# Kernel optimization log

Measured on AMD Instinct MI355X. Metric: run time of the kernel, lower is better.

Reference implementation:

```python
import jax, jax.numpy as jnp
import numpy as np

B, S, D_MODEL = 2, 2048, 1024
NUM_HEADS, ATTN_DIM = 16, 64


def setup_inputs() -> dict:
    key = jax.random.key(0)
    ks = jax.random.split(key, 9)
    scale = 1.0 / np.sqrt(D_MODEL)
    states = jax.random.normal(ks[0], (B, S, D_MODEL), dtype=jnp.float32)
    Wq = jax.random.normal(ks[1], (D_MODEL, NUM_HEADS * ATTN_DIM), dtype=jnp.float32) * scale
    bq = jnp.zeros((NUM_HEADS * ATTN_DIM,), dtype=jnp.float32)
    Wk = jax.random.normal(ks[2], (D_MODEL, NUM_HEADS * ATTN_DIM), dtype=jnp.float32) * scale
    bk = jnp.zeros((NUM_HEADS * ATTN_DIM,), dtype=jnp.float32)
    Wv = jax.random.normal(ks[3], (D_MODEL, NUM_HEADS * ATTN_DIM), dtype=jnp.float32) * scale
    bv = jnp.zeros((NUM_HEADS * ATTN_DIM,), dtype=jnp.float32)
    Wo = jax.random.normal(ks[4], (NUM_HEADS * ATTN_DIM, D_MODEL), dtype=jnp.float32) * scale
    bo = jnp.zeros((D_MODEL,), dtype=jnp.float32)
    return {"states": states, "Wq": Wq, "bq": bq, "Wk": Wk, "bk": bk,
            "Wv": Wv, "bv": bv, "Wo": Wo, "bo": bo}


def reference(states, Wq, bq, Wk, bk, Wv, bv, Wo, bo):
    b, s, _ = states.shape
    h, d = NUM_HEADS, ATTN_DIM

    def proj(W, bias):
        # tanh-activated Dense, then split heads: [b, s, h*d] -> [b, h, s, d]
        y = jnp.tanh(states @ W + bias)
        return y.reshape(b, s, h, d).transpose(0, 2, 1, 3)

    q, k, v = proj(Wq, bq), proj(Wk, bk), proj(Wv, bv)
    # scores: [b, h, s, s]
    alpha = jnp.einsum("bhqd,bhkd->bhqk", q, k) / jnp.sqrt(jnp.float32(d))
    # causal mask (row i attends to cols 0..i); masked logits set to float32.min
    causal = jnp.tril(jnp.ones((s, s), dtype=bool))
    alpha = jnp.where(causal, alpha, jnp.finfo(jnp.float32).min)
    alpha = jax.nn.softmax(alpha, axis=-1)
    ctx = jnp.einsum("bhqk,bhkd->bhqd", alpha, v)  # [b, h, s, d]
    ctx = ctx.transpose(0, 2, 1, 3).reshape(b, s, h * d)
    return jnp.tanh(ctx @ Wo + bo)
```

## Files before the change

kernel.cpp:

```cpp
#include <hip/hip_runtime.h>
#include <math.h>

typedef unsigned short u16;
typedef __attribute__((ext_vector_type(4))) float f32x4;
typedef __attribute__((ext_vector_type(16))) float f32x16;
typedef __attribute__((ext_vector_type(8))) short bf16x8;

#define B_ 2
#define S_ 2048
#define DM 1024
#define H_ 16
#define AD 64
#define ME 4194304
#define SC 0.18033688011112042f
#define SMAX 12.0f

#define GLL(g, s) __builtin_amdgcn_global_load_lds( \
  (const __attribute__((address_space(1))) void*)(g), \
  (__attribute__((address_space(3))) void*)(s), 16, 0, 0)

__device__ inline u16 f2bf(float f) {
  union { float f; unsigned u; } v; v.f = f;
  unsigned r = v.u + 0x7fffu + ((v.u >> 16) & 1u);
  return (u16)(r >> 16);
}

__device__ inline unsigned cvt_pk_bf16(float lo, float hi) {
  unsigned r;
  asm("v_cvt_pk_bf16_f32 %0, %1, %2" : "=v"(r) : "v"(lo), "v"(hi));
  return r;
}

__global__ __launch_bounds__(256) void conv_states(const float* __restrict__ in,
                                                   u16* __restrict__ out) {
  int i = (blockIdx.x * 256 + threadIdx.x) * 8;
  const float4* p = (const float4*)(in + i);
  float4 a = p[0], b = p[1];
  bf16x8 o;
  o[0] = (short)f2bf(a.x); o[1] = (short)f2bf(a.y);
  o[2] = (short)f2bf(a.z); o[3] = (short)f2bf(a.w);
  o[4] = (short)f2bf(b.x); o[5] = (short)f2bf(b.y);
  o[6] = (short)f2bf(b.z); o[7] = (short)f2bf(b.w);
  *(bf16x8*)&out[i] = o;
}

__global__ void transpose_w(const float* __restrict__ Wq, const float* __restrict__ Wk,
                            const float* __restrict__ Wv, const float* __restrict__ Wo,
                            u16* __restrict__ Wt) {
  __shared__ float t[32][33];
  int z = blockIdx.z;
  const float* W = (z == 0) ? Wq : (z == 1) ? Wk : (z == 2) ? Wv : Wo;
  u16* out = Wt + (size_t)z * DM * DM;
  int n0 = blockIdx.x * 32, k0 = blockIdx.y * 32;
  int tx = threadIdx.x, ty = threadIdx.y;
  t[ty][tx] = W[(k0 + ty) * DM + n0 + tx];
  __syncthreads();
  out[(n0 + ty) * DM + k0 + tx] = f2bf(t[tx][ty]);
}

__global__ __launch_bounds__(256) void qkv_gemm(
    const u16* __restrict__ A, const u16* __restrict__ Wt,
    const float* __restrict__ bq, const float* __restrict__ bk, const float* __restrict__ bv,
    u16* __restrict__ Qw, u16* __restrict__ Kw, u16* __restrict__ Vtw) {
  __shared__ __attribute__((aligned(16))) u16 lA[128 * 32];
  __shared__ __attribute__((aligned(16))) u16 lB[128 * 32];
  const int z = blockIdx.z;
  const u16* Bt = Wt + (size_t)z * DM * DM;
  const int m0 = blockIdx.y * 128, n0 = blockIdx.x * 128;
  const int tid = threadIdx.x;
  const int wid = tid >> 6, l = tid & 63;
  const int lr = l & 15, lk = l >> 4;
  const int wm = (wid >> 1) * 64, wn = (wid & 1) * 64;
  const int srow = wid * 32 + (l >> 2);
  const int scol = (l & 3) * 8;

  f32x4 acc[4][4] = {};

  for (int k0 = 0; k0 < DM; k0 += 32) {
    const u16* gA = &A[(size_t)(m0 + srow) * DM + k0 + scol];
    const u16* gB = &Bt[(size_t)(n0 + srow) * DM + k0 + scol];
    GLL(gA,           lA + wid * 1024);
    GLL(gA + 16 * DM, lA + wid * 1024 + 512);
    GLL(gB,           lB + wid * 1024);
    GLL(gB + 16 * DM, lB + wid * 1024 + 512);
    __syncthreads();
    bf16x8 af[4], bfr[4];
#pragma unroll
    for (int g = 0; g < 4; ++g) {
      af[g]  = *(const bf16x8*)&lA[(wm + g * 16 + lr) * 32 + lk * 8];
      bfr[g] = *(const bf16x8*)&lB[(wn + g * 16 + lr) * 32 + lk * 8];
    }
#pragma unroll
    for (int mg = 0; mg < 4; ++mg)
#pragma unroll
      for (int ng = 0; ng < 4; ++ng)
        acc[mg][ng] = __builtin_amdgcn_mfma_f32_16x16x32_bf16(af[mg], bfr[ng], acc[mg][ng], 0, 0, 0);
    __syncthreads();
  }

  const float* bias = (z == 0) ? bq : (z == 1) ? bk : bv;
#pragma unroll
  for (int mg = 0; mg < 4; ++mg)
#pragma unroll
    for (int ng = 0; ng < 4; ++ng)
#pragma unroll
      for (int r = 0; r < 4; ++r) {
        int m = m0 + wm + mg * 16 + lk * 4 + r;
        int n = n0 + wn + ng * 16 + lr;
        float v = tanhf(acc[mg][ng][r] + bias[n]);
        if (z == 0) v *= SC;
        u16 h16 = f2bf(v);
        int bb = m >> 11, s = m & 2047, hh = n >> 6, d = n & 63;
        if (z == 2) Vtw[((size_t)(bb * H_ + hh) * AD + d) * S_ + s] = h16;
        else ((z == 0) ? Qw : Kw)[((size_t)(bb * H_ + hh) * S_ + s) * AD + d] = h16;
      }
}

__global__ __launch_bounds__(256) void out_gemm(
    const u16* __restrict__ A, const u16* __restrict__ Bt,
    const float* __restrict__ bo, float* __restrict__ out) {
  __shared__ __attribute__((aligned(16))) u16 lA[128 * 32];
  __shared__ __attribute__((aligned(16))) u16 lB[128 * 32];
  const int m0 = blockIdx.y * 128, n0 = blockIdx.x * 128;
  const int tid = threadIdx.x;
  const int wid = tid >> 6, l = tid & 63;
  const int lr = l & 15, lk = l >> 4;
  const int wm = (wid >> 1) * 64, wn = (wid & 1) * 64;
  const int srow = wid * 32 + (l >> 2);
  const int scol = (l & 3) * 8;

  f32x4 acc[4][4] = {};

  for (int k0 = 0; k0 < DM; k0 += 32) {
    const u16* gA = &A[(size_t)(m0 + srow) * DM + k0 + scol];
    const u16* gB = &Bt[(size_t)(n0 + srow) * DM + k0 + scol];
    GLL(gA,           lA + wid * 1024);
    GLL(gA + 16 * DM, lA + wid * 1024 + 512);
    GLL(gB,           lB + wid * 1024);
    GLL(gB + 16 * DM, lB + wid * 1024 + 512);
    __syncthreads();
    bf16x8 af[4], bfr[4];
#pragma unroll
    for (int g = 0; g < 4; ++g) {
      af[g]  = *(const bf16x8*)&lA[(wm + g * 16 + lr) * 32 + lk * 8];
      bfr[g] = *(const bf16x8*)&lB[(wn + g * 16 + lr) * 32 + lk * 8];
    }
#pragma unroll
    for (int mg = 0; mg < 4; ++mg)
#pragma unroll
      for (int ng = 0; ng < 4; ++ng)
        acc[mg][ng] = __builtin_amdgcn_mfma_f32_16x16x32_bf16(af[mg], bfr[ng], acc[mg][ng], 0, 0, 0);
    __syncthreads();
  }

#pragma unroll
  for (int mg = 0; mg < 4; ++mg)
#pragma unroll
    for (int ng = 0; ng < 4; ++ng)
#pragma unroll
      for (int r = 0; r < 4; ++r) {
        int m = m0 + wm + mg * 16 + lk * 4 + r;
        int n = n0 + wn + ng * 16 + lr;
        out[(size_t)m * DM + n] = tanhf(acc[mg][ng][r] + bo[n]);
      }
}

__global__ __launch_bounds__(256, 3) void attn_kernel(
    const u16* __restrict__ Q, const u16* __restrict__ K,
    const u16* __restrict__ Vt, u16* __restrict__ ctx,
    float* __restrict__ O0, float* __restrict__ O1, float* __restrict__ O2,
    float* __restrict__ L0, float* __restrict__ L1, float* __restrict__ L2) {
  __shared__ __attribute__((aligned(16))) char smem[32768];
  const int u = blockIdx.x >> 5;
  const int bh = blockIdx.x & 31;
  int t, lo;
  if (u < 11)       { t = u + 5;  lo = 0; }
  else if (u < 16)  { t = u;      lo = 6; }
  else if (u == 16) { t = 4;      lo = 0; }
  else if (u == 17) { t = 10;     lo = 6; }
  else { int r = u - 18, g = r / 3, c = r % 3;
         if (c == 0)      { t = 3 - g;  lo = 0; }
         else if (c == 1) { t = 9 - g;  lo = 6; }
         else             { t = 15 - g; lo = 12; } }
  const int hi = (lo == 0) ? (t < 5 ? t : 5) : ((lo == 6) ? (t < 11 ? t : 11) : t);

  const int tid = threadIdx.x, wl = tid >> 6, l = tid & 63;
  const int lq = l & 31, hl = l >> 5;
  const int q0 = t * 128 + wl * 32;

  const char* Qb = (const char*)(Q + (size_t)bh * S_ * AD);
  const char* Kb = (const char*)(K + (size_t)bh * S_ * AD);
  const char* Vb = (const char*)(Vt + (size_t)bh * AD * S_);

  int kcst[4], vcst[4], ldso[4];
#pragma unroll
  for (int i = 0; i < 4; ++i) {
    int c = wl * 4 + i;
    int o = c * 1024 + l * 16;
    ldso[i] = c * 1024 + l * 16;
    int row = o >> 8;
    int un = (o & 255) ^ ((row & 15) << 4);
    kcst[i] = (row * 2 + (un >> 7)) * 128 + (un & 127);
    vcst[i] = row * (2 * S_) + un;
  }

  bf16x8 qf[4];
#pragma unroll
  for (int ds = 0; ds < 4; ++ds)
    qf[ds] = *(const bf16x8*)(Qb + (size_t)(q0 + lq) * 128 + ds * 32 + hl * 16);

  f32x16 accO[2] = {};
  float lsum = 0.f;

  {
    bf16x8 kr[4], vr[4];
#pragma unroll
    for (int i = 0; i < 4; ++i) {
      kr[i] = *(const bf16x8*)(Kb + (size_t)lo * 16384 + kcst[i]);
      vr[i] = *(const bf16x8*)(Vb + (size_t)lo * 256  + vcst[i]);
    }
#pragma unroll
    for (int i = 0; i < 4; ++i) {
      *(bf16x8*)(smem + ldso[i])         = kr[i];
      *(bf16x8*)(smem + 16384 + ldso[i]) = vr[i];
    }
  }
  __syncthreads();

  const char* kl = smem;
  const char* vl = smem + 16384;

  for (int kb = lo; kb <= hi; ++kb) {
    bf16x8 krn[4], vrn[4];
    const bool pf = (kb < hi);
    if (pf) {
#pragma unroll
      for (int i = 0; i < 4; ++i) {
        krn[i] = *(const bf16x8*)(Kb + (size_t)(kb + 1) * 16384 + kcst[i]);
        vrn[i] = *(const bf16x8*)(Vb + (size_t)(kb + 1) * 256  + vcst[i]);
      }
    }

    const bool diag = (kb == t);
    const int wlim = diag ? wl : 3;

    for (int s = 0; s <= wlim; ++s) {
      f32x16 c = {};
      const int kvl = s * 32 + lq;
      const int rp = kvl >> 1, kbit = kvl & 1;
      const int swz = (rp & 15) << 4;
      __builtin_amdgcn_s_setprio(1);
#pragma unroll
      for (int ds = 0; ds < 4; ++ds) {
        bf16x8 a = *(const bf16x8*)(kl + rp * 256 +
                     (((kbit << 7) | (ds * 32 + hl * 16)) ^ swz));
        c = __builtin_amdgcn_mfma_f32_32x32x16_bf16(a, qf[ds], c, 0, 0, 0);
      }
      __builtin_amdgcn_s_setprio(0);

      const bool tri = diag && (s == wl);
#pragma unroll
      for (int r = 0; r < 16; ++r) {
        float e = __builtin_amdgcn_exp2f(c[r] - SMAX);
        if (tri) {
          int kc = (r & 3) + 8 * (r >> 2) + 4 * hl;
          if (kc > lq) e = 0.f;
        }
        c[r] = e;
        lsum += e;
      }

      unsigned uu[8], su[8];
#pragma unroll
      for (int i = 0; i < 8; ++i) {
        uu[i] = cvt_pk_bf16(c[2 * i], c[2 * i + 1]);
        su[i] = (unsigned)__shfl_xor((int)uu[i], 32);
      }
      union { unsigned w[4]; bf16x8 v; } c0_, c1_;
      c0_.w[0] = hl ? su[2] : uu[0]; c0_.w[1] = hl ? su[3] : uu[1];
      c0_.w[2] = hl ? uu[2] : su[0]; c0_.w[3] = hl ? uu[3] : su[1];
      c1_.w[0] = hl ? su[6] : uu[4]; c1_.w[1] = hl ? su[7] : uu[5];
      c1_.w[2] = hl ? uu[6] : su[4]; c1_.w[3] = hl ? uu[7] : su[5];

      __builtin_amdgcn_s_setprio(1);
#pragma unroll
      for (int d = 0; d < 2; ++d) {
        const int drow = d * 32 + lq;
        const int vswz = (drow & 15) << 4;
        bf16x8 a0 = *(const bf16x8*)(vl + drow * 256 + ((s * 64 + hl * 16) ^ vswz));
        bf16x8 a1 = *(const bf16x8*)(vl + drow * 256 + ((s * 64 + 32 + hl * 16) ^ vswz));
        accO[d] = __builtin_amdgcn_mfma_f32_32x32x16_bf16(a0, c0_.v, accO[d], 0, 0, 0);
        accO[d] = __builtin_amdgcn_mfma_f32_32x32x16_bf16(a1, c1_.v, accO[d], 0, 0, 0);
      }
      __builtin_amdgcn_s_setprio(0);
    }

    __syncthreads();
    if (pf) {
#pragma unroll
      for (int i = 0; i < 4; ++i) {
        *(bf16x8*)(smem + ldso[i])         = krn[i];
        *(bf16x8*)(smem + 16384 + ldso[i]) = vrn[i];
      }
    }
    __syncthreads();
  }

  lsum += __shfl_xor(lsum, 32);
  const int q = q0 + lq;

  if (lo == 0 && t < 6) {
    const float inv = 1.f / lsum;
    u16* cb_ = ctx + ((size_t)(bh >> 4) * S_ + q) * DM + (bh & 15) * AD;
#pragma unroll
    for (int d = 0; d < 2; ++d)
#pragma unroll
      for (int g = 0; g < 4; ++g) {
        unsigned w0 = cvt_pk_bf16(accO[d][4 * g] * inv,     accO[d][4 * g + 1] * inv);
        unsigned w1 = cvt_pk_bf16(accO[d][4 * g + 2] * inv, accO[d][4 * g + 3] * inv);
        unsigned* dst = (unsigned*)(cb_ + d * 32 + 8 * g + 4 * hl);
        dst[0] = w0; dst[1] = w1;
      }
  } else {
    float* Ob; float* Lb;
    if (lo == 0)      { size_t r = (size_t)bh * 1280 + (q - 768);  Ob = O0 + r * 64; Lb = L0 + r; }
    else if (lo == 6) { size_t r = (size_t)bh * 1280 + (q - 768);  Ob = O1 + r * 64; Lb = L1 + r; }
    else              { size_t r = (size_t)bh * 512  + (q - 1536); Ob = O2 + r * 64; Lb = L2 + r; }
#pragma unroll
    for (int d = 0; d < 2; ++d)
#pragma unroll
      for (int g = 0; g < 4; ++g) {
        f32x4 w;
        w[0] = accO[d][4 * g];     w[1] = accO[d][4 * g + 1];
        w[2] = accO[d][4 * g + 2]; w[3] = accO[d][4 * g + 3];
        *(f32x4*)&Ob[d * 32 + 8 * g + 4 * hl] = w;
      }
    if (!hl) *Lb = lsum;
  }
}

__global__ __launch_bounds__(256) void attn_norm(
    const float* __restrict__ O0, const float* __restrict__ O1,
    const float* __restrict__ O2, const float* __restrict__ L0,
    const float* __restrict__ L1, const float* __restrict__ L2,
    u16* __restrict__ ctx) {
  const int tid = threadIdx.x;
  const int rowl = blockIdx.x * 64 + (tid >> 2);
  const int sub = tid & 3;
  const int bh = rowl / 1280, qr = rowl - bh * 1280;
  const int q = 768 + qr;
  float lv = L0[rowl] + L1[rowl];
  const f32x4* p0 = (const f32x4*)(O0 + (size_t)rowl * 64 + sub * 16);
  const f32x4* p1 = (const f32x4*)(O1 + (size_t)rowl * 64 + sub * 16);
  f32x4 v0 = p0[0] + p1[0], v1 = p0[1] + p1[1];
  f32x4 v2 = p0[2] + p1[2], v3 = p0[3] + p1[3];
  if (q >= 1536) {
    size_t r2 = (size_t)bh * 512 + (q - 1536);
    lv += L2[r2];
    const f32x4* p2 = (const f32x4*)(O2 + r2 * 64 + sub * 16);
    v0 += p2[0]; v1 += p2[1]; v2 += p2[2]; v3 += p2[3];
  }
  const float inv = 1.f / lv;
  const int b = bh >> 4, h = bh & 15;
  unsigned w[8];
  w[0] = cvt_pk_bf16(v0[0] * inv, v0[1] * inv);
  w[1] = cvt_pk_bf16(v0[2] * inv, v0[3] * inv);
  w[2] = cvt_pk_bf16(v1[0] * inv, v1[1] * inv);
  w[3] = cvt_pk_bf16(v1[2] * inv, v1[3] * inv);
  w[4] = cvt_pk_bf16(v2[0] * inv, v2[1] * inv);
  w[5] = cvt_pk_bf16(v2[2] * inv, v2[3] * inv);
  w[6] = cvt_pk_bf16(v3[0] * inv, v3[1] * inv);
  w[7] = cvt_pk_bf16(v3[2] * inv, v3[3] * inv);
  unsigned* dst = (unsigned*)(ctx + ((size_t)b * S_ + q) * DM + h * AD + sub * 16);
#pragma unroll
  for (int i = 0; i < 8; ++i) dst[i] = w[i];
}

extern "C" void kernel_launch(void* const* d_in, const int* in_sizes, int n_in,
                              void* d_out, int out_size, void* d_ws, size_t ws_size,
                              hipStream_t stream) {
  const float* states = (const float*)d_in[0];
  const float* Wq = (const float*)d_in[1];
  const float* bq = (const float*)d_in[2];
  const float* Wk = (const float*)d_in[3];
  const float* bk = (const float*)d_in[4];
  const float* Wv = (const float*)d_in[5];
  const float* bv = (const float*)d_in[6];
  const float* Wo = (const float*)d_in[7];
  const float* bo = (const float*)d_in[8];
  float* out = (float*)d_out;

  u16* sbf = (u16*)d_ws;
  u16* wt  = sbf + ME;
  u16* Qw  = wt + ME;
  u16* Kw  = Qw + ME;
  u16* Vtw = Kw + ME;
  u16* ctx = Vtw + ME;
  float* O0 = (float*)(ctx + ME);
  float* O1 = O0 + (size_t)32 * 1280 * 64;
  float* O2 = (float*)d_ws;
  float* L0 = O2 + (size_t)32 * 512 * 64;
  float* L1 = L0 + 32 * 1280;
  float* L2 = L1 + 32 * 1280;

  conv_states<<<ME / (256 * 8), 256, 0, stream>>>(states, sbf);
  transpose_w<<<dim3(32, 32, 4), dim3(32, 32), 0, stream>>>(Wq, Wk, Wv, Wo, wt);
  qkv_gemm<<<dim3(8, 32, 3), 256, 0, stream>>>(sbf, wt, bq, bk, bv, Qw, Kw, Vtw);
  attn_kernel<<<960, 256, 0, stream>>>(Qw, Kw, Vtw, ctx, O0, O1, O2, L0, L1, L2);
  attn_norm<<<640, 256, 0, stream>>>(O0, O1, O2, L0, L1, L2, ctx);
  out_gemm<<<dim3(8, 32), 256, 0, stream>>>(ctx, wt + 3 * (size_t)DM * DM, bo, out);
}
```

Baseline: 130.7 us.

## Widen GEMM K-tiles with swizzled LDS, fast tanh, permlane swap in attention

The QKV and output GEMMs now stage 128-wide K slices (in bytes) with an XOR-swizzled LDS layout, which halves the number of barrier pairs and cuts LDS bank conflicts. The library tanhf in both epilogues is replaced by an exp2/rcp approximation. In attention, the shuffle-and-select exchange of P fragments becomes v_permlane32_swap, and the full (non-diagonal) key blocks run through a fully unrolled inner loop with no masking test. The fast tanh trades a little accuracy for cheaper instructions and may overflow to inf for large inputs, but the result still saturates correctly.

```diff
diff --git a/kernel.cpp b/kernel.cpp
--- a/kernel.cpp
+++ b/kernel.cpp
@@ -29,6 +29,11 @@
   unsigned r;
   asm("v_cvt_pk_bf16_f32 %0, %1, %2" : "=v"(r) : "v"(lo), "v"(hi));
   return r;
+}
+
+__device__ inline float fast_tanh(float x) {
+  float e = __builtin_amdgcn_exp2f(x * 2.885390081777927f);
+  return 1.f - 2.f * __builtin_amdgcn_rcpf(e + 1.f);
 }
 
 __global__ __launch_bounds__(256) void conv_states(const float* __restrict__ in,
@@ -62,39 +67,46 @@
     const u16* __restrict__ A, const u16* __restrict__ Wt,
     const float* __restrict__ bq, const float* __restrict__ bk, const float* __restrict__ bv,
     u16* __restrict__ Qw, u16* __restrict__ Kw, u16* __restrict__ Vtw) {
-  __shared__ __attribute__((aligned(16))) u16 lA[128 * 32];
-  __shared__ __attribute__((aligned(16))) u16 lB[128 * 32];
+  __shared__ __attribute__((aligned(16))) char smem[32768];
   const int z = blockIdx.z;
-  const u16* Bt = Wt + (size_t)z * DM * DM;
   const int m0 = blockIdx.y * 128, n0 = blockIdx.x * 128;
   const int tid = threadIdx.x;
   const int wid = tid >> 6, l = tid & 63;
   const int lr = l & 15, lk = l >> 4;
   const int wm = (wid >> 1) * 64, wn = (wid & 1) * 64;
-  const int srow = wid * 32 + (l >> 2);
-  const int scol = (l & 3) * 8;
+
+  const int srow8 = l >> 3;
+  const int scoff = ((l & 7) ^ srow8) * 16;
+  const char* Ab = (const char*)A;
+  const char* Bb = (const char*)(Wt + (size_t)z * DM * DM);
+  const int rswz = (lr & 7) << 4;
 
   f32x4 acc[4][4] = {};
 
-  for (int k0 = 0; k0 < DM; k0 += 32) {
-    const u16* gA = &A[(size_t)(m0 + srow) * DM + k0 + scol];
-    const u16* gB = &Bt[(size_t)(n0 + srow) * DM + k0 + scol];
-    GLL(gA,           lA + wid * 1024);
-    GLL(gA + 16 * DM, lA + wid * 1024 + 512);
-    GLL(gB,           lB + wid * 1024);
-    GLL(gB + 16 * DM, lB + wid * 1024 + 512);
-    __syncthreads();
-    bf16x8 af[4], bfr[4];
-#pragma unroll
-    for (int g = 0; g < 4; ++g) {
-      af[g]  = *(const bf16x8*)&lA[(wm + g * 16 + lr) * 32 + lk * 8];
-      bfr[g] = *(const bf16x8*)&lB[(wn + g * 16 + lr) * 32 + lk * 8];
-    }
-#pragma unroll
-    for (int mg = 0; mg < 4; ++mg)
-#pragma unroll
-      for (int ng = 0; ng < 4; ++ng)
-        acc[mg][ng] = __builtin_amdgcn_mfma_f32_16x16x32_bf16(af[mg], bfr[ng], acc[mg][ng], 0, 0, 0);
+  for (int kb = 0; kb < 2048; kb += 128) {
+#pragma unroll
+    for (int i = 0; i < 4; ++i) {
+      const int c = wid * 4 + i;
+      const int row = c * 8 + srow8;
+      GLL(Ab + (size_t)(m0 + row) * 2048 + kb + scoff, smem + c * 1024);
+      GLL(Bb + (size_t)(n0 + row) * 2048 + kb + scoff, smem + 16384 + c * 1024);
+    }
+    __syncthreads();
+#pragma unroll
+    for (int ks = 0; ks < 2; ++ks) {
+      const int koff = (ks * 64 + lk * 16) ^ rswz;
+      bf16x8 af[4], bfr[4];
+#pragma unroll
+      for (int g = 0; g < 4; ++g) {
+        af[g]  = *(const bf16x8*)(smem + (wm + g * 16 + lr) * 128 + koff);
+        bfr[g] = *(const bf16x8*)(smem + 16384 + (wn + g * 16 + lr) * 128 + koff);
+      }
+#pragma unroll
+      for (int mg = 0; mg < 4; ++mg)
+#pragma unroll
+        for (int ng = 0; ng < 4; ++ng)
+          acc[mg][ng] = __builtin_amdgcn_mfma_f32_16x16x32_bf16(af[mg], bfr[ng], acc[mg][ng], 0, 0, 0);
+    }
     __syncthreads();
   }
 
@@ -107,7 +119,7 @@
       for (int r = 0; r < 4; ++r) {
         int m = m0 + wm + mg * 16 + lk * 4 + r;
         int n = n0 + wn + ng * 16 + lr;
-        float v = tanhf(acc[mg][ng][r] + bias[n]);
+        float v = fast_tanh(acc[mg][ng][r] + bias[n]);
         if (z == 0) v *= SC;
         u16 h16 = f2bf(v);
         int bb = m >> 11, s = m & 2047, hh = n >> 6, d = n & 63;
@@ -119,37 +131,45 @@
 __global__ __launch_bounds__(256) void out_gemm(
     const u16* __restrict__ A, const u16* __restrict__ Bt,
     const float* __restrict__ bo, float* __restrict__ out) {
-  __shared__ __attribute__((aligned(16))) u16 lA[128 * 32];
-  __shared__ __attribute__((aligned(16))) u16 lB[128 * 32];
+  __shared__ __attribute__((aligned(16))) char smem[32768];
   const int m0 = blockIdx.y * 128, n0 = blockIdx.x * 128;
   const int tid = threadIdx.x;
   const int wid = tid >> 6, l = tid & 63;
   const int lr = l & 15, lk = l >> 4;
   const int wm = (wid >> 1) * 64, wn = (wid & 1) * 64;
-  const int srow = wid * 32 + (l >> 2);
-  const int scol = (l & 3) * 8;
+
+  const int srow8 = l >> 3;
+  const int scoff = ((l & 7) ^ srow8) * 16;
+  const char* Ab = (const char*)A;
+  const char* Bb = (const char*)Bt;
+  const int rswz = (lr & 7) << 4;
 
   f32x4 acc[4][4] = {};
 
-  for (int k0 = 0; k0 < DM; k0 += 32) {
-    const u16* gA = &A[(size_t)(m0 + srow) * DM + k0 + scol];
-    const u16* gB = &Bt[(size_t)(n0 + srow) * DM + k0 + scol];
-    GLL(gA,           lA + wid * 1024);
-    GLL(gA + 16 * DM, lA + wid * 1024 + 512);
-    GLL(gB,           lB + wid * 1024);
-    GLL(gB + 16 * DM, lB + wid * 1024 + 512);
-    __syncthreads();
-    bf16x8 af[4], bfr[4];
-#pragma unroll
-    for (int g = 0; g < 4; ++g) {
-      af[g]  = *(const bf16x8*)&lA[(wm + g * 16 + lr) * 32 + lk * 8];
-      bfr[g] = *(const bf16x8*)&lB[(wn + g * 16 + lr) * 32 + lk * 8];
-    }
-#pragma unroll
-    for (int mg = 0; mg < 4; ++mg)
-#pragma unroll
-      for (int ng = 0; ng < 4; ++ng)
-        acc[mg][ng] = __builtin_amdgcn_mfma_f32_16x16x32_bf16(af[mg], bfr[ng], acc[mg][ng], 0, 0, 0);
+  for (int kb = 0; kb < 2048; kb += 128) {
+#pragma unroll
+    for (int i = 0; i < 4; ++i) {
+      const int c = wid * 4 + i;
+      const int row = c * 8 + srow8;
+      GLL(Ab + (size_t)(m0 + row) * 2048 + kb + scoff, smem + c * 1024);
+      GLL(Bb + (size_t)(n0 + row) * 2048 + kb + scoff, smem + 16384 + c * 1024);
+    }
+    __syncthreads();
+#pragma unroll
+    for (int ks = 0; ks < 2; ++ks) {
+      const int koff = (ks * 64 + lk * 16) ^ rswz;
+      bf16x8 af[4], bfr[4];
+#pragma unroll
+      for (int g = 0; g < 4; ++g) {
+        af[g]  = *(const bf16x8*)(smem + (wm + g * 16 + lr) * 128 + koff);
+        bfr[g] = *(const bf16x8*)(smem + 16384 + (wn + g * 16 + lr) * 128 + koff);
+      }
+#pragma unroll
+      for (int mg = 0; mg < 4; ++mg)
+#pragma unroll
+        for (int ng = 0; ng < 4; ++ng)
+          acc[mg][ng] = __builtin_amdgcn_mfma_f32_16x16x32_bf16(af[mg], bfr[ng], acc[mg][ng], 0, 0, 0);
+    }
     __syncthreads();
   }
 
@@ -161,7 +181,7 @@
       for (int r = 0; r < 4; ++r) {
         int m = m0 + wm + mg * 16 + lk * 4 + r;
         int n = n0 + wn + ng * 16 + lr;
-        out[(size_t)m * DM + n] = tanhf(acc[mg][ng][r] + bo[n]);
+        out[(size_t)m * DM + n] = fast_tanh(acc[mg][ng][r] + bo[n]);
       }
 }
 
@@ -230,6 +250,60 @@
   const char* kl = smem;
   const char* vl = smem + 16384;
 
+  auto sblock = [&](int s, bool tri) {
+    f32x16 c = {};
+    const int kvl = s * 32 + lq;
+    const int rp = kvl >> 1, kbit = kvl & 1;
+    const int swz = (rp & 15) << 4;
+    __builtin_amdgcn_s_setprio(1);
+#pragma unroll
+    for (int ds = 0; ds < 4; ++ds) {
+      bf16x8 a = *(const bf16x8*)(kl + rp * 256 +
+                   (((kbit << 7) | (ds * 32 + hl * 16)) ^ swz));
+      c = __builtin_amdgcn_mfma_f32_32x32x16_bf16(a, qf[ds], c, 0, 0, 0);
+    }
+    __builtin_amdgcn_s_setprio(0);
+
+#pragma unroll
+    for (int r = 0; r < 16; ++r) {
+      float e = __builtin_amdgcn_exp2f(c[r] - SMAX);
+      if (tri) {
+        int kc = (r & 3) + 8 * (r >> 2) + 4 * hl;
+        if (kc > lq) e = 0.f;
+      }
+      c[r] = e;
+      lsum += e;
+    }
+
+    unsigned uu[8];
+#pragma unroll
+    for (int i = 0; i < 8; ++i)
+      uu[i] = cvt_pk_bf16(c[2 * i], c[2 * i + 1]);
+    unsigned s0a = uu[0], s0b = uu[2];
+    unsigned s1a = uu[1], s1b = uu[3];
+    unsigned s2a = uu[4], s2b = uu[6];
+    unsigned s3a = uu[5], s3b = uu[7];
+    asm("v_permlane32_swap_b32 %0, %1" : "+v"(s0a), "+v"(s0b));
+    asm("v_permlane32_swap_b32 %0, %1" : "+v"(s1a), "+v"(s1b));
+    asm("v_permlane32_swap_b32 %0, %1" : "+v"(s2a), "+v"(s2b));
+    asm("v_permlane32_swap_b32 %0, %1" : "+v"(s3a), "+v"(s3b));
+    union { unsigned w[4]; bf16x8 v; } c0_, c1_;
+    c0_.w[0] = s0a; c0_.w[1] = s1a; c0_.w[2] = s0b; c0_.w[3] = s1b;
+    c1_.w[0] = s2a; c1_.w[1] = s3a; c1_.w[2] = s2b; c1_.w[3] = s3b;
+
+    __builtin_amdgcn_s_setprio(1);
+#pragma unroll
+    for (int d = 0; d < 2; ++d) {
+      const int drow = d * 32 + lq;
+      const int vswz = (drow & 15) << 4;
+      bf16x8 a0 = *(const bf16x8*)(vl + drow * 256 + ((s * 64 + hl * 16) ^ vswz));
+      bf16x8 a1 = *(const bf16x8*)(vl + drow * 256 + ((s * 64 + 32 + hl * 16) ^ vswz));
+      accO[d] = __builtin_amdgcn_mfma_f32_32x32x16_bf16(a0, c0_.v, accO[d], 0, 0, 0);
+      accO[d] = __builtin_amdgcn_mfma_f32_32x32x16_bf16(a1, c1_.v, accO[d], 0, 0, 0);
+    }
+    __builtin_amdgcn_s_setprio(0);
+  };
+
   for (int kb = lo; kb <= hi; ++kb) {
     bf16x8 krn[4], vrn[4];
     const bool pf = (kb < hi);
@@ -241,58 +315,12 @@
       }
     }
 
-    const bool diag = (kb == t);
-    const int wlim = diag ? wl : 3;
-
-    for (int s = 0; s <= wlim; ++s) {
-      f32x16 c = {};
-      const int kvl = s * 32 + lq;
-      const int rp = kvl >> 1, kbit = kvl & 1;
-      const int swz = (rp & 15) << 4;
-      __builtin_amdgcn_s_setprio(1);
-#pragma unroll
-      for (int ds = 0; ds < 4; ++ds) {
-        bf16x8 a = *(const bf16x8*)(kl + rp * 256 +
-                     (((kbit << 7) | (ds * 32 + hl * 16)) ^ swz));
-        c = __builtin_amdgcn_mfma_f32_32x32x16_bf16(a, qf[ds], c, 0, 0, 0);
-      }
-      __builtin_amdgcn_s_setprio(0);
-
-      const bool tri = diag && (s == wl);
-#pragma unroll
-      for (int r = 0; r < 16; ++r) {
-        float e = __builtin_amdgcn_exp2f(c[r] - SMAX);
-        if (tri) {
-          int kc = (r & 3) + 8 * (r >> 2) + 4 * hl;
-          if (kc > lq) e = 0.f;
-        }
-        c[r] = e;
-        lsum += e;
-      }
-
-      unsigned uu[8], su[8];
-#pragma unroll
-      for (int i = 0; i < 8; ++i) {
-        uu[i] = cvt_pk_bf16(c[2 * i], c[2 * i + 1]);
-        su[i] = (unsigned)__shfl_xor((int)uu[i], 32);
-      }
-      union { unsigned w[4]; bf16x8 v; } c0_, c1_;
-      c0_.w[0] = hl ? su[2] : uu[0]; c0_.w[1] = hl ? su[3] : uu[1];
-      c0_.w[2] = hl ? uu[2] : su[0]; c0_.w[3] = hl ? uu[3] : su[1];
-      c1_.w[0] = hl ? su[6] : uu[4]; c1_.w[1] = hl ? su[7] : uu[5];
-      c1_.w[2] = hl ? uu[6] : su[4]; c1_.w[3] = hl ? uu[7] : su[5];
-
-      __builtin_amdgcn_s_setprio(1);
-#pragma unroll
-      for (int d = 0; d < 2; ++d) {
-        const int drow = d * 32 + lq;
-        const int vswz = (drow & 15) << 4;
-        bf16x8 a0 = *(const bf16x8*)(vl + drow * 256 + ((s * 64 + hl * 16) ^ vswz));
-        bf16x8 a1 = *(const bf16x8*)(vl + drow * 256 + ((s * 64 + 32 + hl * 16) ^ vswz));
-        accO[d] = __builtin_amdgcn_mfma_f32_32x32x16_bf16(a0, c0_.v, accO[d], 0, 0, 0);
-        accO[d] = __builtin_amdgcn_mfma_f32_32x32x16_bf16(a1, c1_.v, accO[d], 0, 0, 0);
-      }
-      __builtin_amdgcn_s_setprio(0);
+    if (kb != t) {
+#pragma unroll
+      for (int s = 0; s < 4; ++s) sblock(s, false);
+    } else {
+      for (int s = 0; s < wl; ++s) sblock(s, false);
+      sblock(wl, true);
     }
 
     __syncthreads();
```

New measurement: 131.3 us. Within noise of the previous version (+0.5%).
